# Kernel tuning notes

Measured on AMD Instinct MI355X. Metric: run time of the kernel, lower is better.

The kernel has to match this reference:

```python
import jax, jax.numpy as jnp
import numpy as np

NUM_ADAPTIVE = 8
WEIGHT_ALPHA = 1.0


def setup_inputs() -> dict:
    key = jax.random.key(0)
    k1, k2, k3, k4 = jax.random.split(key, 4)
    B, C, S = 128, 4, 65536
    inp = jax.random.normal(k1, (B, C, S), dtype=jnp.float32)
    target = jax.random.randint(k2, (B, S), 0, C, dtype=jnp.int64)
    adaptive_target = jax.random.randint(k3, (B, S), 0, NUM_ADAPTIVE, dtype=jnp.int64)
    mask = jax.random.randint(k4, (B, S), 0, 2).astype(jnp.float32)
    return {"input": inp, "target": target, "adaptive_target": adaptive_target, "mask": mask}


def reference(input, target, adaptive_target, mask):
    # Per-position cross entropy, reduction='none'. input: (B, C, S)
    logp = jax.nn.log_softmax(input, axis=1)                      # (B, C, S)
    ce = -jnp.take_along_axis(logp, target[:, None, :], axis=1)[:, 0, :]  # (B, S)

    loss = ce * mask                                              # masked per-position loss
    valid = (mask > 0).astype(loss.dtype)                         # (B, S)

    # Per-adaptive-class masked mean loss via a single segment reduction
    seg = adaptive_target.reshape(-1).astype(jnp.int32)
    class_sum = jax.ops.segment_sum((loss * valid).reshape(-1), seg, num_segments=NUM_ADAPTIVE)
    class_cnt = jax.ops.segment_sum(valid.reshape(-1), seg, num_segments=NUM_ADAPTIVE)

    fallback = jnp.mean(loss)                                     # loss.mean() in the original
    has = class_cnt > 0
    class_losses = jnp.where(has, class_sum / jnp.where(has, class_cnt, 1.0), fallback)
    class_counts = jnp.where(has, class_cnt, 1.0)

    total = jnp.sum(class_losses * class_counts)
    props = jnp.where(total > 0,
                      class_losses * class_counts / jnp.where(total > 0, total, 1.0),
                      jnp.full((NUM_ADAPTIVE,), 1.0 / NUM_ADAPTIVE, dtype=loss.dtype))
    class_weights = 1.0 + WEIGHT_ALPHA * props                    # (8,)

    adaptive_weights = class_weights[adaptive_target]             # gather back to (B, S)
    final_loss = jnp.sum(loss * adaptive_weights) / jnp.sum(mask)
    return final_loss
```

## Files before the change

### kernel.cpp

```cpp
#include <hip/hip_runtime.h>

constexpr int B = 128;
constexpr int C = 4;
constexpr int S = 65536;
constexpr int N = B * S;
constexpr int NG = N / 4;
constexpr int NSEG = 8;
constexpr int NACC = 2 * NSEG;

constexpr int GRID = 8192;
constexpr int BLOCK = 256;
static_assert(GRID * BLOCK == NG, "one float4 group per thread");


__global__ __launch_bounds__(BLOCK) void ce_partial_kernel(
    const float* __restrict__ input,
    const int*   __restrict__ target,
    const int*   __restrict__ seg,
    const float* __restrict__ mask,
    float* __restrict__ pt)
{
    const int g = blockIdx.x * BLOCK + threadIdx.x;
    const int p = g << 2;
    const int b = p >> 16;
    const int s = p & (S - 1);
    const int base = (b << 18) + s;

    const float4 l0 = *(const float4*)(input + base);
    const float4 l1 = *(const float4*)(input + base + S);
    const float4 l2 = *(const float4*)(input + base + 2 * S);
    const float4 l3 = *(const float4*)(input + base + 3 * S);
    const int4   tg = *(const int4*)(target + p);
    const int4   sv = *(const int4*)(seg + p);
    const float4 mk = *(const float4*)(mask + p);

    float ssum[NSEG], scnt[NSEG];
#pragma unroll
    for (int k = 0; k < NSEG; ++k) { ssum[k] = 0.f; scnt[k] = 0.f; }

    const float a0[4] = { l0.x, l0.y, l0.z, l0.w };
    const float a1[4] = { l1.x, l1.y, l1.z, l1.w };
    const float a2[4] = { l2.x, l2.y, l2.z, l2.w };
    const float a3[4] = { l3.x, l3.y, l3.z, l3.w };
    const int   tgv[4] = { tg.x, tg.y, tg.z, tg.w };
    const int   sgv[4] = { sv.x, sv.y, sv.z, sv.w };
    const float mkv[4] = { mk.x, mk.y, mk.z, mk.w };

#pragma unroll
    for (int j = 0; j < 4; ++j) {
        const float x0 = a0[j], x1 = a1[j], x2 = a2[j], x3 = a3[j];
        const float m = fmaxf(fmaxf(x0, x1), fmaxf(x2, x3));
        const float sum = __expf(x0 - m) + __expf(x1 - m)
                        + __expf(x2 - m) + __expf(x3 - m);
        const float lse = m + __logf(sum);
        const int t = tgv[j];
        const float chosen = (t == 0) ? x0 : (t == 1) ? x1 : (t == 2) ? x2 : x3;
        const float mval = mkv[j];
        const float loss = (lse - chosen) * mval;
        const int sgj = sgv[j];
#pragma unroll
        for (int k = 0; k < NSEG; ++k) {
            const bool hit = (sgj == k);
            ssum[k] += hit ? loss : 0.f;
            scnt[k] += hit ? mval : 0.f;
        }
    }

    float vals[NACC];
#pragma unroll
    for (int k = 0; k < NSEG; ++k) { vals[k] = ssum[k]; vals[NSEG + k] = scnt[k]; }
#pragma unroll
    for (int i = 0; i < NACC; ++i) {
        float v = vals[i];
#pragma unroll
        for (int off = 32; off > 0; off >>= 1)
            v += __shfl_xor(v, off, 64);
        vals[i] = v;
    }

    __shared__ float red[4][NACC];
    const int wave = threadIdx.x >> 6;
    const int lane = threadIdx.x & 63;
    if (lane == 0) {
#pragma unroll
        for (int i = 0; i < NACC; ++i) red[wave][i] = vals[i];
    }
    __syncthreads();
    if (threadIdx.x < NACC) {
        const int i = threadIdx.x;
        pt[i * GRID + blockIdx.x] =
            red[0][i] + red[1][i] + red[2][i] + red[3][i];
    }
}

__global__ __launch_bounds__(1024) void ce_final_kernel(
    const float* __restrict__ pt, float* __restrict__ out)
{
    const int t = threadIdx.x;
    float vals[NACC];
#pragma unroll
    for (int i = 0; i < NACC; ++i) {
        float v = 0.f;
#pragma unroll
        for (int k = 0; k < GRID / 1024; ++k)
            v += pt[i * GRID + t + k * 1024];
#pragma unroll
        for (int off = 32; off > 0; off >>= 1)
            v += __shfl_xor(v, off, 64);
        vals[i] = v;
    }

    __shared__ float red[16][NACC];
    const int wave = t >> 6;
    const int lane = t & 63;
    if (lane == 0) {
#pragma unroll
        for (int i = 0; i < NACC; ++i) red[wave][i] = vals[i];
    }
    __syncthreads();

    if (t == 0) {
        float acc[NACC];
        for (int i = 0; i < NACC; ++i) {
            float v = 0.f;
            for (int w = 0; w < 16; ++w) v += red[w][i];
            acc[i] = v;
        }

        float ssum[NSEG], scnt[NSEG];
        float tot_loss = 0.f, msum = 0.f;
        for (int k = 0; k < NSEG; ++k) {
            ssum[k] = acc[k];
            scnt[k] = acc[NSEG + k];
            tot_loss += ssum[k];
            msum += scnt[k];
        }
        const float fallback = tot_loss / (float)N;

        float cl[NSEG], cc[NSEG];
        float total = 0.f;
        for (int k = 0; k < NSEG; ++k) {
            const bool has = scnt[k] > 0.f;
            cl[k] = has ? (ssum[k] / scnt[k]) : fallback;
            cc[k] = has ? scnt[k] : 1.f;
            total += cl[k] * cc[k];
        }
        float num = 0.f;
        for (int k = 0; k < NSEG; ++k) {
            const float prop = (total > 0.f) ? (cl[k] * cc[k] / total)
                                             : (1.f / (float)NSEG);
            const float w = 1.f + prop;
            num += w * ssum[k];
        }
        out[0] = num / msum;
    }
}

extern "C" void kernel_launch(void* const* d_in, const int* in_sizes, int n_in,
                              void* d_out, int out_size, void* d_ws, size_t ws_size,
                              hipStream_t stream) {
    const float* input  = (const float*)d_in[0];
    const int*   target = (const int*)d_in[1];
    const int*   seg    = (const int*)d_in[2];
    const float* mask   = (const float*)d_in[3];
    float* pt  = (float*)d_ws;
    float* out = (float*)d_out;

    ce_partial_kernel<<<GRID, BLOCK, 0, stream>>>(input, target, seg, mask, pt);
    ce_final_kernel<<<1, 1024, 0, stream>>>(pt, out);
}
```

Baseline: 267.7 us.

## Use persistent grid-stride loop with register prefetch and nontemporal loads

Cuts the grid from 8192 to 1024 blocks, so each thread handles eight float4 groups in a loop and prefetches the next group's loads into registers while computing the current one. Loads now use nontemporal hints to avoid polluting cache with streamed data. The per-thread 16-value shuffle reduction and partial-result writes now happen once per eight groups, and the final kernel reads fewer partials. The risk is lower occupancy and higher register pressure from double-buffering seven vectors, which may reduce memory-level parallelism on a purely bandwidth-bound kernel.

```diff
diff --git a/kernel.cpp b/kernel.cpp
--- a/kernel.cpp
+++ b/kernel.cpp
@@ -8,10 +8,38 @@
 constexpr int NSEG = 8;
 constexpr int NACC = 2 * NSEG;
 
-constexpr int GRID = 8192;
+constexpr int GRID = 1024;
 constexpr int BLOCK = 256;
-static_assert(GRID * BLOCK == NG, "one float4 group per thread");
+constexpr int ITERS = 8;
+static_assert(GRID * BLOCK * ITERS == NG, "exact tiling");
 
+typedef float fx4 __attribute__((ext_vector_type(4)));
+typedef int   ix4 __attribute__((ext_vector_type(4)));
+
+struct Grp {
+    fx4 l0, l1, l2, l3;
+    ix4 tg, sv;
+    fx4 mk;
+};
+
+__device__ __forceinline__ Grp load_grp(
+    const float* __restrict__ input, const int* __restrict__ target,
+    const int* __restrict__ seg, const float* __restrict__ mask, int g)
+{
+    const int p = g << 2;
+    const int b = p >> 16;
+    const int s = p & (S - 1);
+    const int base = (b << 18) + s;
+    Grp r;
+    r.l0 = __builtin_nontemporal_load((const fx4*)(input + base));
+    r.l1 = __builtin_nontemporal_load((const fx4*)(input + base + S));
+    r.l2 = __builtin_nontemporal_load((const fx4*)(input + base + 2 * S));
+    r.l3 = __builtin_nontemporal_load((const fx4*)(input + base + 3 * S));
+    r.tg = __builtin_nontemporal_load((const ix4*)(target + p));
+    r.sv = __builtin_nontemporal_load((const ix4*)(seg + p));
+    r.mk = __builtin_nontemporal_load((const fx4*)(mask + p));
+    return r;
+}
 
 __global__ __launch_bounds__(BLOCK) void ce_partial_kernel(
     const float* __restrict__ input,
@@ -20,50 +48,48 @@
     const float* __restrict__ mask,
     float* __restrict__ pt)
 {
-    const int g = blockIdx.x * BLOCK + threadIdx.x;
-    const int p = g << 2;
-    const int b = p >> 16;
-    const int s = p & (S - 1);
-    const int base = (b << 18) + s;
-
-    const float4 l0 = *(const float4*)(input + base);
-    const float4 l1 = *(const float4*)(input + base + S);
-    const float4 l2 = *(const float4*)(input + base + 2 * S);
-    const float4 l3 = *(const float4*)(input + base + 3 * S);
-    const int4   tg = *(const int4*)(target + p);
-    const int4   sv = *(const int4*)(seg + p);
-    const float4 mk = *(const float4*)(mask + p);
-
     float ssum[NSEG], scnt[NSEG];
 #pragma unroll
     for (int k = 0; k < NSEG; ++k) { ssum[k] = 0.f; scnt[k] = 0.f; }
 
-    const float a0[4] = { l0.x, l0.y, l0.z, l0.w };
-    const float a1[4] = { l1.x, l1.y, l1.z, l1.w };
-    const float a2[4] = { l2.x, l2.y, l2.z, l2.w };
-    const float a3[4] = { l3.x, l3.y, l3.z, l3.w };
-    const int   tgv[4] = { tg.x, tg.y, tg.z, tg.w };
-    const int   sgv[4] = { sv.x, sv.y, sv.z, sv.w };
-    const float mkv[4] = { mk.x, mk.y, mk.z, mk.w };
+    const int g0 = blockIdx.x * BLOCK + threadIdx.x;
+    constexpr int STEP = GRID * BLOCK;
+
+    Grp cur = load_grp(input, target, seg, mask, g0);
+#pragma unroll 1
+    for (int it = 0; it < ITERS; ++it) {
+        Grp nxt;
+        if (it + 1 < ITERS)
+            nxt = load_grp(input, target, seg, mask, g0 + (it + 1) * STEP);
+
+        const float a0[4] = { cur.l0.x, cur.l0.y, cur.l0.z, cur.l0.w };
+        const float a1[4] = { cur.l1.x, cur.l1.y, cur.l1.z, cur.l1.w };
+        const float a2[4] = { cur.l2.x, cur.l2.y, cur.l2.z, cur.l2.w };
+        const float a3[4] = { cur.l3.x, cur.l3.y, cur.l3.z, cur.l3.w };
+        const int   tgv[4] = { cur.tg.x, cur.tg.y, cur.tg.z, cur.tg.w };
+        const int   sgv[4] = { cur.sv.x, cur.sv.y, cur.sv.z, cur.sv.w };
+        const float mkv[4] = { cur.mk.x, cur.mk.y, cur.mk.z, cur.mk.w };
 
 #pragma unroll
-    for (int j = 0; j < 4; ++j) {
-        const float x0 = a0[j], x1 = a1[j], x2 = a2[j], x3 = a3[j];
-        const float m = fmaxf(fmaxf(x0, x1), fmaxf(x2, x3));
-        const float sum = __expf(x0 - m) + __expf(x1 - m)
-                        + __expf(x2 - m) + __expf(x3 - m);
-        const float lse = m + __logf(sum);
-        const int t = tgv[j];
-        const float chosen = (t == 0) ? x0 : (t == 1) ? x1 : (t == 2) ? x2 : x3;
-        const float mval = mkv[j];
-        const float loss = (lse - chosen) * mval;
-        const int sgj = sgv[j];
+        for (int j = 0; j < 4; ++j) {
+            const float x0 = a0[j], x1 = a1[j], x2 = a2[j], x3 = a3[j];
+            const float m = fmaxf(fmaxf(x0, x1), fmaxf(x2, x3));
+            const float sum = __expf(x0 - m) + __expf(x1 - m)
+                            + __expf(x2 - m) + __expf(x3 - m);
+            const float lse = m + __logf(sum);
+            const int t = tgv[j];
+            const float chosen = (t == 0) ? x0 : (t == 1) ? x1 : (t == 2) ? x2 : x3;
+            const float mval = mkv[j];
+            const float loss = (lse - chosen) * mval;
+            const int sgj = sgv[j];
 #pragma unroll
-        for (int k = 0; k < NSEG; ++k) {
-            const bool hit = (sgj == k);
-            ssum[k] += hit ? loss : 0.f;
-            scnt[k] += hit ? mval : 0.f;
+            for (int k = 0; k < NSEG; ++k) {
+                const bool hit = (sgj == k);
+                ssum[k] += hit ? loss : 0.f;
+                scnt[k] += hit ? mval : 0.f;
+            }
         }
+        cur = nxt;
     }
 
     float vals[NACC];
@@ -100,10 +126,7 @@
     float vals[NACC];
 #pragma unroll
     for (int i = 0; i < NACC; ++i) {
-        float v = 0.f;
-#pragma unroll
-        for (int k = 0; k < GRID / 1024; ++k)
-            v += pt[i * GRID + t + k * 1024];
+        float v = pt[i * GRID + t];
 #pragma unroll
         for (int off = 32; off > 0; off >>= 1)
             v += __shfl_xor(v, off, 64);
```

After: 246.8 us. 7.8% less time.

## Persistent waves with double-buffered global-to-LDS async loads

Applied to the files above, without the earlier changes.

Shrinks the grid to 512 persistent blocks. Each wave loops over 16 tiles and prefetches the next tile directly into LDS with global_load_lds while it computes the current one, waiting with an explicit vmcnt. The aim is to keep more memory requests in flight per wave and to cut block launch and partial-reduction overhead. The final reduction shrinks to match. The cost is lower parallelism, since fewer waves are resident, and a dependence on hand-written waitcnt correctness.

```diff
diff --git a/kernel.cpp b/kernel.cpp
--- a/kernel.cpp
+++ b/kernel.cpp
@@ -8,10 +8,43 @@
 constexpr int NSEG = 8;
 constexpr int NACC = 2 * NSEG;
 
-constexpr int GRID = 8192;
+constexpr int GRID  = 512;
 constexpr int BLOCK = 256;
-static_assert(GRID * BLOCK == NG, "one float4 group per thread");
-
+constexpr int WAVES = BLOCK / 64;
+constexpr int NWAVE = GRID * WAVES;
+constexpr int TILES = NG / (NWAVE * 64);
+static_assert(TILES * NWAVE * 64 == NG, "exact tiling");
+
+constexpr int SEGB  = 1024;
+constexpr int TILEB = 7 * SEGB;
+constexpr int DEPTH = 2;
+
+typedef float fx4 __attribute__((ext_vector_type(4)));
+typedef int   ix4 __attribute__((ext_vector_type(4)));
+
+#define GLB(p) ((const __attribute__((address_space(1))) void*)(p))
+#define LDS(p) ((__attribute__((address_space(3))) void*)(p))
+
+__device__ __forceinline__ void issue_tile(
+    const float* __restrict__ input, const int* __restrict__ target,
+    const int* __restrict__ seg, const float* __restrict__ mask,
+    char* lb, int wave_id, int t, int lane)
+{
+    const int g0 = (wave_id + t * NWAVE) * 64;
+    const int p0 = g0 << 2;
+    const int b  = p0 >> 16;
+    const int s  = p0 & (S - 1);
+    const int base = (b << 18) + s;
+    const int lo = lane * 16;
+
+    __builtin_amdgcn_global_load_lds(GLB((const char*)(input + base)         + lo), LDS(lb + 0 * SEGB), 16, 0, 0);
+    __builtin_amdgcn_global_load_lds(GLB((const char*)(input + base +     S) + lo), LDS(lb + 1 * SEGB), 16, 0, 0);
+    __builtin_amdgcn_global_load_lds(GLB((const char*)(input + base + 2 * S) + lo), LDS(lb + 2 * SEGB), 16, 0, 0);
+    __builtin_amdgcn_global_load_lds(GLB((const char*)(input + base + 3 * S) + lo), LDS(lb + 3 * SEGB), 16, 0, 0);
+    __builtin_amdgcn_global_load_lds(GLB((const char*)(target + p0)          + lo), LDS(lb + 4 * SEGB), 16, 0, 0);
+    __builtin_amdgcn_global_load_lds(GLB((const char*)(seg    + p0)          + lo), LDS(lb + 5 * SEGB), 16, 0, 0);
+    __builtin_amdgcn_global_load_lds(GLB((const char*)(mask   + p0)          + lo), LDS(lb + 6 * SEGB), 16, 0, 0);
+}
 
 __global__ __launch_bounds__(BLOCK) void ce_partial_kernel(
     const float* __restrict__ input,
@@ -20,49 +53,66 @@
     const float* __restrict__ mask,
     float* __restrict__ pt)
 {
-    const int g = blockIdx.x * BLOCK + threadIdx.x;
-    const int p = g << 2;
-    const int b = p >> 16;
-    const int s = p & (S - 1);
-    const int base = (b << 18) + s;
-
-    const float4 l0 = *(const float4*)(input + base);
-    const float4 l1 = *(const float4*)(input + base + S);
-    const float4 l2 = *(const float4*)(input + base + 2 * S);
-    const float4 l3 = *(const float4*)(input + base + 3 * S);
-    const int4   tg = *(const int4*)(target + p);
-    const int4   sv = *(const int4*)(seg + p);
-    const float4 mk = *(const float4*)(mask + p);
+    __shared__ __align__(16) char smem[WAVES * DEPTH * TILEB];
+    __shared__ float red[WAVES][NACC];
+
+    const int lane = threadIdx.x & 63;
+    const int w    = threadIdx.x >> 6;
+    const int wave_id = blockIdx.x * WAVES + w;
+    char* mybuf = smem + w * (DEPTH * TILEB);
 
     float ssum[NSEG], scnt[NSEG];
 #pragma unroll
     for (int k = 0; k < NSEG; ++k) { ssum[k] = 0.f; scnt[k] = 0.f; }
 
-    const float a0[4] = { l0.x, l0.y, l0.z, l0.w };
-    const float a1[4] = { l1.x, l1.y, l1.z, l1.w };
-    const float a2[4] = { l2.x, l2.y, l2.z, l2.w };
-    const float a3[4] = { l3.x, l3.y, l3.z, l3.w };
-    const int   tgv[4] = { tg.x, tg.y, tg.z, tg.w };
-    const int   sgv[4] = { sv.x, sv.y, sv.z, sv.w };
-    const float mkv[4] = { mk.x, mk.y, mk.z, mk.w };
-
-#pragma unroll
-    for (int j = 0; j < 4; ++j) {
-        const float x0 = a0[j], x1 = a1[j], x2 = a2[j], x3 = a3[j];
-        const float m = fmaxf(fmaxf(x0, x1), fmaxf(x2, x3));
-        const float sum = __expf(x0 - m) + __expf(x1 - m)
-                        + __expf(x2 - m) + __expf(x3 - m);
-        const float lse = m + __logf(sum);
-        const int t = tgv[j];
-        const float chosen = (t == 0) ? x0 : (t == 1) ? x1 : (t == 2) ? x2 : x3;
-        const float mval = mkv[j];
-        const float loss = (lse - chosen) * mval;
-        const int sgj = sgv[j];
-#pragma unroll
-        for (int k = 0; k < NSEG; ++k) {
-            const bool hit = (sgj == k);
-            ssum[k] += hit ? loss : 0.f;
-            scnt[k] += hit ? mval : 0.f;
+    issue_tile(input, target, seg, mask, mybuf, wave_id, 0, lane);
+
+#pragma unroll 1
+    for (int t = 0; t < TILES; ++t) {
+        if (t + 1 < TILES) {
+            issue_tile(input, target, seg, mask,
+                       mybuf + ((t + 1) & 1) * TILEB, wave_id, t + 1, lane);
+            asm volatile("s_waitcnt vmcnt(7)" ::: "memory");
+        } else {
+            asm volatile("s_waitcnt vmcnt(0)" ::: "memory");
+        }
+
+        const char* lb = mybuf + (t & 1) * TILEB;
+        const int lo = lane * 16;
+        const fx4 l0 = *(const fx4*)(lb + 0 * SEGB + lo);
+        const fx4 l1 = *(const fx4*)(lb + 1 * SEGB + lo);
+        const fx4 l2 = *(const fx4*)(lb + 2 * SEGB + lo);
+        const fx4 l3 = *(const fx4*)(lb + 3 * SEGB + lo);
+        const ix4 tg = *(const ix4*)(lb + 4 * SEGB + lo);
+        const ix4 sv = *(const ix4*)(lb + 5 * SEGB + lo);
+        const fx4 mk = *(const fx4*)(lb + 6 * SEGB + lo);
+
+        const float a0[4] = { l0.x, l0.y, l0.z, l0.w };
+        const float a1[4] = { l1.x, l1.y, l1.z, l1.w };
+        const float a2[4] = { l2.x, l2.y, l2.z, l2.w };
+        const float a3[4] = { l3.x, l3.y, l3.z, l3.w };
+        const int   tgv[4] = { tg.x, tg.y, tg.z, tg.w };
+        const int   sgv[4] = { sv.x, sv.y, sv.z, sv.w };
+        const float mkv[4] = { mk.x, mk.y, mk.z, mk.w };
+
+#pragma unroll
+        for (int j = 0; j < 4; ++j) {
+            const float x0 = a0[j], x1 = a1[j], x2 = a2[j], x3 = a3[j];
+            const float m = fmaxf(fmaxf(x0, x1), fmaxf(x2, x3));
+            const float sum = __expf(x0 - m) + __expf(x1 - m)
+                            + __expf(x2 - m) + __expf(x3 - m);
+            const float lse = m + __logf(sum);
+            const int tt = tgv[j];
+            const float chosen = (tt == 0) ? x0 : (tt == 1) ? x1 : (tt == 2) ? x2 : x3;
+            const float mval = mkv[j];
+            const float loss = (lse - chosen) * mval;
+            const int sgj = sgv[j];
+#pragma unroll
+            for (int k = 0; k < NSEG; ++k) {
+                const bool hit = (sgj == k);
+                ssum[k] += hit ? loss : 0.f;
+                scnt[k] += hit ? mval : 0.f;
+            }
         }
     }
 
@@ -78,12 +128,9 @@
         vals[i] = v;
     }
 
-    __shared__ float red[4][NACC];
-    const int wave = threadIdx.x >> 6;
-    const int lane = threadIdx.x & 63;
     if (lane == 0) {
 #pragma unroll
-        for (int i = 0; i < NACC; ++i) red[wave][i] = vals[i];
+        for (int i = 0; i < NACC; ++i) red[w][i] = vals[i];
     }
     __syncthreads();
     if (threadIdx.x < NACC) {
@@ -93,24 +140,21 @@
     }
 }
 
-__global__ __launch_bounds__(1024) void ce_final_kernel(
+__global__ __launch_bounds__(512) void ce_final_kernel(
     const float* __restrict__ pt, float* __restrict__ out)
 {
     const int t = threadIdx.x;
     float vals[NACC];
 #pragma unroll
     for (int i = 0; i < NACC; ++i) {
-        float v = 0.f;
-#pragma unroll
-        for (int k = 0; k < GRID / 1024; ++k)
-            v += pt[i * GRID + t + k * 1024];
+        float v = pt[i * GRID + t];
 #pragma unroll
         for (int off = 32; off > 0; off >>= 1)
             v += __shfl_xor(v, off, 64);
         vals[i] = v;
     }
 
-    __shared__ float red[16][NACC];
+    __shared__ float red[8][NACC];
     const int wave = t >> 6;
     const int lane = t & 63;
     if (lane == 0) {
@@ -123,7 +167,7 @@
         float acc[NACC];
         for (int i = 0; i < NACC; ++i) {
             float v = 0.f;
-            for (int w = 0; w < 16; ++w) v += red[w][i];
+            for (int w = 0; w < 8; ++w) v += red[w][i];
             acc[i] = v;
         }
 
@@ -167,5 +211,5 @@
     float* out = (float*)d_out;
 
     ce_partial_kernel<<<GRID, BLOCK, 0, stream>>>(input, target, seg, mask, pt);
-    ce_final_kernel<<<1, 1024, 0, stream>>>(pt, out);
-}
+    ce_final_kernel<<<1, 512, 0, stream>>>(pt, out);
+}
```

Result: no change. 264.1 us (-1.3%).
